# Kernel tuning notes

Measured on AMD Instinct MI355X. Metric: run time of the kernel, lower is better.

Reference implementation:

```python
import jax, jax.numpy as jnp
import numpy as np

NEG_SLOPE = 0.2  # negative_slope of LeakyReLU in GATConv
N_NODES = 50000
N_EDGES = 800000
R = 2
IN_DIM = 128
HID = 32
HEADS = 4
OUT = 32


def setup_inputs() -> dict:
    key = jax.random.key(0)
    ks = jax.random.split(key, 12)
    s = 0.1  # keep pre-activations tame
    x = jax.random.normal(ks[0], (N_NODES, IN_DIM), dtype=jnp.float32)
    W1 = jax.random.normal(ks[1], (R, IN_DIM, HEADS * HID), dtype=jnp.float32) * s
    al1 = jax.random.normal(ks[2], (R, HEADS, HID), dtype=jnp.float32) * s
    ar1 = jax.random.normal(ks[3], (R, HEADS, HID), dtype=jnp.float32) * s
    b1 = jax.random.normal(ks[4], (R, HEADS * HID), dtype=jnp.float32) * s
    W2 = jax.random.normal(ks[5], (R, HEADS * HID, HEADS * OUT), dtype=jnp.float32) * s
    al2 = jax.random.normal(ks[6], (R, HEADS, OUT), dtype=jnp.float32) * s
    ar2 = jax.random.normal(ks[7], (R, HEADS, OUT), dtype=jnp.float32) * s
    b2 = jax.random.normal(ks[8], (R, HEADS * OUT), dtype=jnp.float32) * s
    edges = jax.random.randint(ks[9], (R, 2, N_EDGES), 0, N_NODES, dtype=jnp.int32)
    return {"x": x, "W1": W1, "al1": al1, "ar1": ar1, "b1": b1,
            "W2": W2, "al2": al2, "ar2": ar2, "b2": b2, "edges": edges}


def _gat_rel(h, W, al, ar, src, dst, n):
    """Single-relation GATConv aggregation (no bias/residual/activation)."""
    H, D = al.shape
    feat = (h @ W).reshape(n, H, D)                   # [N,H,D]
    el = jnp.einsum('nhd,hd->nh', feat, al)           # [N,H]
    er = jnp.einsum('nhd,hd->nh', feat, ar)
    e = el[src] + er[dst]                             # [E,H]
    e = jnp.where(e > 0, e, NEG_SLOPE * e)            # LeakyReLU
    # edge softmax over incoming edges of each dst node (numerically stable)
    m = jax.ops.segment_max(e, dst, num_segments=n)
    ex = jnp.exp(e - m[dst])
    denom = jax.ops.segment_sum(ex, dst, num_segments=n)
    alpha = ex / jnp.maximum(denom[dst], 1e-9)        # [E,H]
    msg = alpha[:, :, None] * feat[src]               # [E,H,D]
    return jax.ops.segment_sum(msg, dst, num_segments=n)  # [N,H,D]


def reference(x, W1, al1, ar1, b1, W2, al2, ar2, b2, edges):
    n = x.shape[0]
    r_count = edges.shape[0]
    H1, D1 = al1.shape[1:]
    # --- layer 1: per-relation GATConv (bias + elu inside), sum across relations
    acc = jnp.zeros((n, H1, D1), dtype=x.dtype)
    for r in range(r_count):
        src, dst = edges[r, 0], edges[r, 1]
        o = _gat_rel(x, W1[r], al1[r], ar1[r], src, dst, n)
        acc = acc + jax.nn.elu(o + b1[r].reshape(1, H1, D1))
    h = acc.reshape(n, H1 * D1)                       # flatten heads
    # --- layer 2: residual (identity, since in == heads*out), bias, no activation
    H2, D2 = al2.shape[1:]
    res = h.reshape(n, H2, D2)
    acc2 = jnp.zeros((n, H2, D2), dtype=x.dtype)
    for r in range(r_count):
        src, dst = edges[r, 0], edges[r, 1]
        o = _gat_rel(h, W2[r], al2[r], ar2[r], src, dst, n)
        acc2 = acc2 + o + res + b2[r].reshape(1, H2, D2)
    return acc2.mean(axis=1)                          # mean over heads -> [N, OUT]
```

## Files before the change

### kernel.cpp

```cpp
#include <hip/hip_runtime.h>
#include <math.h>

#define HEADS 4
#define DIM 32
#define FDIM 128
#define EPB 8192
#define BPBSH 8

typedef __attribute__((ext_vector_type(8))) short short8;
typedef __attribute__((ext_vector_type(16))) float float16;

__device__ __forceinline__ unsigned short f2bf(float x) {
  unsigned u = __float_as_uint(x);
  u += 0x7FFFu + ((u >> 16) & 1);
  return (unsigned short)(u >> 16);
}

__global__ void convw_kernel(const float* __restrict__ W1, const float* __restrict__ W2,
                             unsigned short* __restrict__ WT, int R) {
  int idx = blockIdx.x * 256 + threadIdx.x;
  if (idx >= 2 * R * FDIM * FDIM) return;
  int lr = idx >> 14;
  int rem = idx & 16383;
  int n = rem >> 7, k = rem & 127;
  const float* W = (lr < R) ? (W1 + (size_t)lr * FDIM * FDIM)
                            : (W2 + (size_t)(lr - R) * FDIM * FDIM);
  WT[idx] = f2bf(W[k * FDIM + n]);
}

__global__ __launch_bounds__(256) void binA_kernel(const int* __restrict__ edges,
                                                   int* __restrict__ cntA, int E, int BA) {
  __shared__ int hist[256];
  int r = blockIdx.y, blk = blockIdx.x, t = threadIdx.x;
  hist[t] = 0;
  __syncthreads();
  const int* dst = edges + (size_t)r * 2 * E + E;
  int base = blk * EPB;
#pragma unroll
  for (int j = 0; j < EPB / 256; ++j) {
    int e = base + t + j * 256;
    if (e < E) atomicAdd(&hist[dst[e] >> BPBSH], 1);
  }
  __syncthreads();
  cntA[((size_t)r * BA + blk) * 256 + t] = hist[t];
}

__global__ __launch_bounds__(256) void scanA_kernel(int* __restrict__ cntA,
                                                    int* __restrict__ bucketBase,
                                                    int E, int NB, int BA) {
  __shared__ int tot[256];
  __shared__ int basep[257];
  int r = blockIdx.x, b = threadIdx.x;
  int run = 0;
  if (b < NB) {
    for (int blk = 0; blk < BA; ++blk) {
      size_t idx = ((size_t)r * BA + blk) * 256 + b;
      int c = cntA[idx];
      cntA[idx] = run;
      run += c;
    }
  }
  tot[b] = (b < NB) ? run : 0;
  __syncthreads();
  if (b == 0) {
    int acc = 0;
    for (int i = 0; i < NB; ++i) { basep[i] = acc; acc += tot[i]; }
    basep[NB] = acc;
  }
  __syncthreads();
  if (b <= NB) bucketBase[r * 257 + b] = basep[b];
  if (b < NB) {
    int bb = basep[b];
    for (int blk = 0; blk < BA; ++blk)
      cntA[((size_t)r * BA + blk) * 256 + b] += bb;
  }
}

__global__ __launch_bounds__(256) void scatterA_kernel(const int* __restrict__ edges,
    const int* __restrict__ cntA, int2* __restrict__ binned, int E, int BA) {
  __shared__ int cur[256];
  int r = blockIdx.y, blk = blockIdx.x, t = threadIdx.x;
  cur[t] = cntA[((size_t)r * BA + blk) * 256 + t];
  __syncthreads();
  const int* srcp = edges + (size_t)r * 2 * E;
  const int* dstp = srcp + E;
  int2* bout = binned + (size_t)r * E;
  int base = blk * EPB;
#pragma unroll
  for (int j = 0; j < EPB / 256; ++j) {
    int e = base + t + j * 256;
    if (e < E) {
      int d = dstp[e], s = srcp[e];
      int pos = atomicAdd(&cur[d >> BPBSH], 1);
      bout[pos] = make_int2(d, s);
    }
  }
}

__global__ __launch_bounds__(256) void passB_kernel(const int2* __restrict__ binned,
    const int* __restrict__ bucketBase, int* __restrict__ csr, int* __restrict__ indptr,
    int E, int N, int NB) {
  __shared__ int cnt[256];
  __shared__ int off[256];
  __shared__ int cur[256];
  int r = blockIdx.y, b = blockIdx.x, t = threadIdx.x;
  int beg = bucketBase[r * 257 + b];
  int end = bucketBase[r * 257 + b + 1];
  cnt[t] = 0;
  __syncthreads();
  const int2* bin = binned + (size_t)r * E;
  for (int i = beg + t; i < end; i += 256)
    atomicAdd(&cnt[bin[i].x & 255], 1);
  __syncthreads();
  for (int ofs = 1; ofs < 256; ofs <<= 1) {
    int u = (t >= ofs) ? cnt[t - ofs] : 0;
    __syncthreads();
    cnt[t] += u;
    __syncthreads();
  }
  int ex = beg + ((t > 0) ? cnt[t - 1] : 0);
  off[t] = ex;
  cur[t] = ex;
  __syncthreads();
  int node = b * 256 + t;
  if (node < N) indptr[(size_t)r * (N + 1) + node] = off[t];
  if (b == NB - 1 && t == 0) indptr[(size_t)r * (N + 1) + N] = E;
  int* csr_r = csr + (size_t)r * E;
  for (int i = beg + t; i < end; i += 256) {
    int2 p = bin[i];
    int rank = atomicAdd(&cur[p.x & 255], 1);
    csr_r[rank] = p.y;
  }
}

__global__ __launch_bounds__(256) void mm_kernel(const float* __restrict__ A,
    const unsigned short* __restrict__ WTl, const float* __restrict__ al_all,
    const float* __restrict__ ar_all, unsigned short* __restrict__ featb_all,
    float* __restrict__ el_all, float* __restrict__ er_all, int N) {
  __shared__ unsigned short sA[128 * 136];
  __shared__ float sAl[FDIM], sAr[FDIM];
  int r = blockIdx.y;
  const unsigned short* WT = WTl + (size_t)r * FDIM * FDIM;
  int row0 = blockIdx.x * 128;
  int t = threadIdx.x;
  if (t < FDIM) {
    sAl[t] = al_all[r * FDIM + t];
    sAr[t] = ar_all[r * FDIM + t];
  }
#pragma unroll
  for (int it = 0; it < 16; ++it) {
    int idx = t * 4 + it * 1024;
    int row = idx >> 7, k = idx & 127;
    int grow = row0 + row;
    float4 v = make_float4(0.f, 0.f, 0.f, 0.f);
    if (grow < N) v = *(const float4*)(A + (size_t)grow * FDIM + k);
    unsigned short* p = sA + row * 136 + k;
    p[0] = f2bf(v.x); p[1] = f2bf(v.y); p[2] = f2bf(v.z); p[3] = f2bf(v.w);
  }
  __syncthreads();
  int lane = t & 63, w = t >> 6;
  int m = lane & 31, q = lane >> 5;
  float16 acc[4] = {0.f, 0.f, 0.f, 0.f};
#pragma unroll
  for (int kc = 0; kc < 8; ++kc) {
    int ko = kc * 16 + q * 8;
    short8 a = *(const short8*)(sA + (w * 32 + m) * 136 + ko);
#pragma unroll
    for (int nt = 0; nt < 4; ++nt) {
      short8 bb = *(const short8*)(WT + (size_t)(nt * 32 + m) * FDIM + ko);
      acc[nt] = __builtin_amdgcn_mfma_f32_32x32x16_bf16(a, bb, acc[nt], 0, 0, 0);
    }
  }
  __syncthreads();
#pragma unroll
  for (int nt = 0; nt < 4; ++nt) {
#pragma unroll
    for (int reg = 0; reg < 16; ++reg) {
      int rr = (reg & 3) + 8 * (reg >> 2) + 4 * q;
      sA[(w * 32 + rr) * 136 + nt * 32 + m] = f2bf(acc[nt][reg]);
    }
  }
  __syncthreads();
  unsigned short* fb = featb_all + (size_t)r * N * FDIM;
#pragma unroll
  for (int it = 0; it < 8; ++it) {
    int idx = (t + it * 256) * 8;
    int row = idx >> 7, k = idx & 127;
    int grow = row0 + row;
    if (grow < N)
      *(uint4*)(fb + (size_t)grow * FDIM + k) = *(const uint4*)(sA + row * 136 + k);
  }
  int rowc = t >> 1, grow = row0 + rowc;
  if (grow < N) {
    float* elr = el_all + (size_t)r * N * 4;
    float* err_ = er_all + (size_t)r * N * 4;
#pragma unroll
    for (int hh = 0; hh < 2; ++hh) {
      int hd = (t & 1) * 2 + hh;
      const uint4* rp4 = (const uint4*)(sA + rowc * 136 + hd * DIM);
      const float4* alp = (const float4*)(sAl + hd * DIM);
      const float4* arp = (const float4*)(sAr + hd * DIM);
      float sl = 0.f, sr = 0.f;
#pragma unroll
      for (int gq = 0; gq < 4; ++gq) {
        uint4 u = rp4[gq];
        float4 a0 = alp[2 * gq], a1 = alp[2 * gq + 1];
        float4 r0 = arp[2 * gq], r1 = arp[2 * gq + 1];
        unsigned uv[4] = {u.x, u.y, u.z, u.w};
        float fv[8];
#pragma unroll
        for (int j = 0; j < 4; ++j) {
          fv[2 * j] = __uint_as_float(uv[j] << 16);
          fv[2 * j + 1] = __uint_as_float(uv[j] & 0xFFFF0000u);
        }
        sl = fmaf(fv[0], a0.x, sl); sr = fmaf(fv[0], r0.x, sr);
        sl = fmaf(fv[1], a0.y, sl); sr = fmaf(fv[1], r0.y, sr);
        sl = fmaf(fv[2], a0.z, sl); sr = fmaf(fv[2], r0.z, sr);
        sl = fmaf(fv[3], a0.w, sl); sr = fmaf(fv[3], r0.w, sr);
        sl = fmaf(fv[4], a1.x, sl); sr = fmaf(fv[4], r1.x, sr);
        sl = fmaf(fv[5], a1.y, sl); sr = fmaf(fv[5], r1.y, sr);
        sl = fmaf(fv[6], a1.z, sl); sr = fmaf(fv[6], r1.z, sr);
        sl = fmaf(fv[7], a1.w, sl); sr = fmaf(fv[7], r1.w, sr);
      }
      elr[(size_t)grow * 4 + hd] = sl;
      err_[(size_t)grow * 4 + hd] = sr;
    }
  }
}

__global__ __launch_bounds__(256) void agg1_kernel(const unsigned short* __restrict__ featb,
    const float* __restrict__ el, const float* __restrict__ er,
    const int* __restrict__ indptr, const int* __restrict__ csr,
    const float* __restrict__ bias, float* __restrict__ hout, int N, int E, int R) {
  int t = blockIdx.x * 256 + threadIdx.x;
  int node = t >> 3;
  if (node >= N) return;
  int hd = t & 3, sub = (t >> 2) & 1;
  float tot[32];
#pragma unroll
  for (int i = 0; i < 32; ++i) tot[i] = 0.f;
  for (int r = 0; r < R; ++r) {
    const unsigned short* f = featb + (size_t)r * N * FDIM + hd * DIM;
    const float* elr = el + (size_t)r * N * 4;
    const int* csr_r = csr + (size_t)r * E;
    const int* ip = indptr + (size_t)r * (N + 1);
    float er_h = er[(size_t)r * N * 4 + node * 4 + hd];
    int beg = ip[node], end = ip[node + 1];
    float l = 0.f, a[32];
#pragma unroll
    for (int i = 0; i < 32; ++i) a[i] = 0.f;
    for (int i = beg + sub; i < end; i += 2) {
      int s = csr_r[i];
      float ee = elr[s * 4 + hd] + er_h;
      ee = ee > 0.f ? ee : 0.2f * ee;
      float p = __expf(ee);
      const uint4* fp = (const uint4*)(f + (size_t)s * FDIM);
      uint4 u0 = fp[0], u1 = fp[1], u2 = fp[2], u3 = fp[3];
      l += p;
      unsigned uu[16] = {u0.x, u0.y, u0.z, u0.w, u1.x, u1.y, u1.z, u1.w,
                         u2.x, u2.y, u2.z, u2.w, u3.x, u3.y, u3.z, u3.w};
#pragma unroll
      for (int j = 0; j < 16; ++j) {
        float f0 = __uint_as_float(uu[j] << 16);
        float f1 = __uint_as_float(uu[j] & 0xFFFF0000u);
        a[2 * j]     = fmaf(p, f0, a[2 * j]);
        a[2 * j + 1] = fmaf(p, f1, a[2 * j + 1]);
      }
    }
    l += __shfl_xor(l, 4);
#pragma unroll
    for (int i = 0; i < 32; ++i) a[i] += __shfl_xor(a[i], 4);
    float inv = (l > 0.f) ? 1.f / l : 0.f;
    const float4* b4 = (const float4*)(bias + r * FDIM + hd * DIM);
#pragma unroll
    for (int g = 0; g < 8; ++g) {
      float4 bv = b4[g];
      float v0 = a[4 * g] * inv + bv.x;
      float v1 = a[4 * g + 1] * inv + bv.y;
      float v2 = a[4 * g + 2] * inv + bv.z;
      float v3 = a[4 * g + 3] * inv + bv.w;
      tot[4 * g]     += v0 > 0.f ? v0 : __expf(v0) - 1.f;
      tot[4 * g + 1] += v1 > 0.f ? v1 : __expf(v1) - 1.f;
      tot[4 * g + 2] += v2 > 0.f ? v2 : __expf(v2) - 1.f;
      tot[4 * g + 3] += v3 > 0.f ? v3 : __expf(v3) - 1.f;
    }
  }
  if (sub == 0) {
    float4* hp = (float4*)(hout + (size_t)node * FDIM + hd * DIM);
#pragma unroll
    for (int g = 0; g < 8; ++g)
      hp[g] = make_float4(tot[4 * g], tot[4 * g + 1], tot[4 * g + 2], tot[4 * g + 3]);
  }
}

__global__ __launch_bounds__(256) void agg2_kernel(const unsigned short* __restrict__ featb,
    const float* __restrict__ el, const float* __restrict__ er,
    const int* __restrict__ indptr, const int* __restrict__ csr,
    const float* __restrict__ bias, const float* __restrict__ hf,
    float* __restrict__ out, int N, int E, int R) {
  int t = blockIdx.x * 256 + threadIdx.x;
  int node = t >> 3;
  if (node >= N) return;
  int hd = t & 3, sub = (t >> 2) & 1;
  float tot[32];
#pragma unroll
  for (int i = 0; i < 32; ++i) tot[i] = 0.f;
  for (int r = 0; r < R; ++r) {
    const unsigned short* f = featb + (size_t)r * N * FDIM + hd * DIM;
    const float* elr = el + (size_t)r * N * 4;
    const int* csr_r = csr + (size_t)r * E;
    const int* ip = indptr + (size_t)r * (N + 1);
    float er_h = er[(size_t)r * N * 4 + node * 4 + hd];
    int beg = ip[node], end = ip[node + 1];
    float l = 0.f, a[32];
#pragma unroll
    for (int i = 0; i < 32; ++i) a[i] = 0.f;
    for (int i = beg + sub; i < end; i += 2) {
      int s = csr_r[i];
      float ee = elr[s * 4 + hd] + er_h;
      ee = ee > 0.f ? ee : 0.2f * ee;
      float p = __expf(ee);
      const uint4* fp = (const uint4*)(f + (size_t)s * FDIM);
      uint4 u0 = fp[0], u1 = fp[1], u2 = fp[2], u3 = fp[3];
      l += p;
      unsigned uu[16] = {u0.x, u0.y, u0.z, u0.w, u1.x, u1.y, u1.z, u1.w,
                         u2.x, u2.y, u2.z, u2.w, u3.x, u3.y, u3.z, u3.w};
#pragma unroll
      for (int j = 0; j < 16; ++j) {
        float f0 = __uint_as_float(uu[j] << 16);
        float f1 = __uint_as_float(uu[j] & 0xFFFF0000u);
        a[2 * j]     = fmaf(p, f0, a[2 * j]);
        a[2 * j + 1] = fmaf(p, f1, a[2 * j + 1]);
      }
    }
    l += __shfl_xor(l, 4);
#pragma unroll
    for (int i = 0; i < 32; ++i) a[i] += __shfl_xor(a[i], 4);
    float inv = (l > 0.f) ? 1.f / l : 0.f;
    const float4* b4 = (const float4*)(bias + r * FDIM + hd * DIM);
#pragma unroll
    for (int g = 0; g < 8; ++g) {
      float4 bv = b4[g];
      tot[4 * g]     += a[4 * g] * inv + bv.x;
      tot[4 * g + 1] += a[4 * g + 1] * inv + bv.y;
      tot[4 * g + 2] += a[4 * g + 2] * inv + bv.z;
      tot[4 * g + 3] += a[4 * g + 3] * inv + bv.w;
    }
  }
  {
    const float4* rv4 = (const float4*)(hf + (size_t)node * FDIM + hd * DIM);
#pragma unroll
    for (int g = 0; g < 8; ++g) {
      float4 rv = rv4[g];
      tot[4 * g]     += R * rv.x;
      tot[4 * g + 1] += R * rv.y;
      tot[4 * g + 2] += R * rv.z;
      tot[4 * g + 3] += R * rv.w;
    }
  }
#pragma unroll
  for (int i = 0; i < 32; ++i) {
    float v = tot[i];
    v += __shfl_xor(v, 1);
    v += __shfl_xor(v, 2);
    tot[i] = v * 0.25f;
  }
  if (sub == 0) {
    float4* op = (float4*)(out + (size_t)node * 32 + hd * 8);
    op[0] = make_float4(tot[hd * 8], tot[hd * 8 + 1], tot[hd * 8 + 2], tot[hd * 8 + 3]);
    op[1] = make_float4(tot[hd * 8 + 4], tot[hd * 8 + 5], tot[hd * 8 + 6], tot[hd * 8 + 7]);
  }
}

extern "C" void kernel_launch(void* const* d_in, const int* in_sizes, int n_in,
                              void* d_out, int out_size, void* d_ws, size_t ws_size,
                              hipStream_t stream) {
  const float* x   = (const float*)d_in[0];
  const float* W1  = (const float*)d_in[1];
  const float* al1 = (const float*)d_in[2];
  const float* ar1 = (const float*)d_in[3];
  const float* b1  = (const float*)d_in[4];
  const float* W2  = (const float*)d_in[5];
  const float* al2 = (const float*)d_in[6];
  const float* ar2 = (const float*)d_in[7];
  const float* b2  = (const float*)d_in[8];
  const int* edges = (const int*)d_in[9];
  float* out = (float*)d_out;

  const int N = in_sizes[0] / FDIM;
  const int R = in_sizes[1] / (FDIM * FDIM);
  const int E = in_sizes[9] / (2 * R);
  const int BA = (E + EPB - 1) / EPB;
  const int NB = (N + 255) >> BPBSH;

  char* ws = (char*)d_ws;
  size_t off = 0;
  auto alloc = [&](size_t bytes) {
    char* p = ws + off;
    off += (bytes + 255) & ~(size_t)255;
    return p;
  };
  unsigned short* featb = (unsigned short*)alloc((size_t)R * N * FDIM * 2);
  unsigned short* WT    = (unsigned short*)alloc((size_t)2 * R * FDIM * FDIM * 2);
  float* el = (float*)alloc((size_t)R * N * 4 * 4);
  float* er = (float*)alloc((size_t)R * N * 4 * 4);
  float* h  = (float*)alloc((size_t)N * FDIM * 4);
  int* cntA = (int*)alloc((size_t)R * BA * 256 * 4);
  int* bucketBase = (int*)alloc((size_t)R * 257 * 4);
  int2* binned = (int2*)alloc((size_t)R * E * 8);
  int* csr = (int*)alloc((size_t)R * E * 4);
  int* indptr = (int*)alloc((size_t)R * (N + 1) * 4);

  convw_kernel<<<(2 * R * FDIM * FDIM + 255) / 256, 256, 0, stream>>>(W1, W2, WT, R);
  dim3 bgrid(BA, R);
  binA_kernel<<<bgrid, 256, 0, stream>>>(edges, cntA, E, BA);
  scanA_kernel<<<R, 256, 0, stream>>>(cntA, bucketBase, E, NB, BA);
  scatterA_kernel<<<bgrid, 256, 0, stream>>>(edges, cntA, binned, E, BA);
  dim3 pgrid(NB, R);
  passB_kernel<<<pgrid, 256, 0, stream>>>(binned, bucketBase, csr, indptr, E, N, NB);

  dim3 mmgrid((N + 127) / 128, R);
  int agrid = (N * 8 + 255) / 256;

  mm_kernel<<<mmgrid, 256, 0, stream>>>(x, WT, al1, ar1, featb, el, er, N);
  agg1_kernel<<<agrid, 256, 0, stream>>>(featb, el, er, indptr, csr, b1, h, N, E, R);

  mm_kernel<<<mmgrid, 256, 0, stream>>>(h, WT + (size_t)R * FDIM * FDIM, al2, ar2, featb, el, er, N);
  agg2_kernel<<<agrid, 256, 0, stream>>>(featb, el, er, indptr, csr, b2, h, out, N, E, R);
}
```

Measured before the change: 377.7 us.

## Widen aggregation to 4 edge lanes per head, fuse weight conversion into binning

The aggregation kernels now use 16 threads per node instead of 8, so each head's incoming edges are split over 4 lanes, with an extra shuffle-reduction step. The aim is more parallelism and more gathers in flight for the latency-bound edge loop. The weight transpose and bf16 conversion is folded into extra blocks of the binning kernel, which removes one launch. The count table is transposed to a per-bucket row layout so the scan can read rows contiguously and use a parallel prefix sum instead of a serial loop. The cost is twice as many threads each holding 32-float accumulators, plus more shuffles.

New measurement: 387.1 us. 1.02x slower.

```diff
diff --git a/kernel.cpp b/kernel.cpp
--- a/kernel.cpp
+++ b/kernel.cpp
@@ -6,6 +6,7 @@
 #define FDIM 128
 #define EPB 8192
 #define BPBSH 8
+#define WB 16
 
 typedef __attribute__((ext_vector_type(8))) short short8;
 typedef __attribute__((ext_vector_type(16))) float float16;
@@ -16,22 +17,26 @@
   return (unsigned short)(u >> 16);
 }
 
-__global__ void convw_kernel(const float* __restrict__ W1, const float* __restrict__ W2,
-                             unsigned short* __restrict__ WT, int R) {
-  int idx = blockIdx.x * 256 + threadIdx.x;
-  if (idx >= 2 * R * FDIM * FDIM) return;
-  int lr = idx >> 14;
-  int rem = idx & 16383;
-  int n = rem >> 7, k = rem & 127;
-  const float* W = (lr < R) ? (W1 + (size_t)lr * FDIM * FDIM)
-                            : (W2 + (size_t)(lr - R) * FDIM * FDIM);
-  WT[idx] = f2bf(W[k * FDIM + n]);
-}
-
 __global__ __launch_bounds__(256) void binA_kernel(const int* __restrict__ edges,
-                                                   int* __restrict__ cntA, int E, int BA) {
+    int* __restrict__ cntA, const float* __restrict__ W1, const float* __restrict__ W2,
+    unsigned short* __restrict__ WT, int E, int BA, int BAp, int R) {
+  int r = blockIdx.y, blk = blockIdx.x, t = threadIdx.x;
+  if (blk >= BA) {
+    int wb = blk - BA;
+    int base = wb * (32768 / WB);
+#pragma unroll
+    for (int j = 0; j < 32768 / WB; j += 256) {
+      int idx = base + j + t;
+      int layer = idx >> 14;
+      int rem = idx & 16383;
+      int n = rem >> 7, k = rem & 127;
+      const float* W = layer ? (W2 + (size_t)r * FDIM * FDIM)
+                             : (W1 + (size_t)r * FDIM * FDIM);
+      WT[((size_t)(layer * R + r) << 14) + rem] = f2bf(W[k * FDIM + n]);
+    }
+    return;
+  }
   __shared__ int hist[256];
-  int r = blockIdx.y, blk = blockIdx.x, t = threadIdx.x;
   hist[t] = 0;
   __syncthreads();
   const int* dst = edges + (size_t)r * 2 * E + E;
@@ -42,45 +47,43 @@
     if (e < E) atomicAdd(&hist[dst[e] >> BPBSH], 1);
   }
   __syncthreads();
-  cntA[((size_t)r * BA + blk) * 256 + t] = hist[t];
+  cntA[((size_t)r * 256 + t) * BAp + blk] = hist[t];
 }
 
 __global__ __launch_bounds__(256) void scanA_kernel(int* __restrict__ cntA,
-                                                    int* __restrict__ bucketBase,
-                                                    int E, int NB, int BA) {
-  __shared__ int tot[256];
-  __shared__ int basep[257];
+    int* __restrict__ bucketBase, int E, int NB, int BA, int BAp) {
+  __shared__ int stot[256];
   int r = blockIdx.x, b = threadIdx.x;
-  int run = 0;
+  int* row = cntA + ((size_t)r * 256 + b) * BAp;
+  int tot = 0;
+  if (b < NB)
+    for (int blk = 0; blk < BA; ++blk) tot += row[blk];
+  stot[b] = tot;
+  __syncthreads();
+  for (int ofs = 1; ofs < 256; ofs <<= 1) {
+    int u = (b >= ofs) ? stot[b - ofs] : 0;
+    __syncthreads();
+    stot[b] += u;
+    __syncthreads();
+  }
+  int excl = stot[b] - tot;
+  if (b < NB) bucketBase[r * 257 + b] = excl;
+  if (b == 0) bucketBase[r * 257 + NB] = E;
   if (b < NB) {
+    int run = excl;
     for (int blk = 0; blk < BA; ++blk) {
-      size_t idx = ((size_t)r * BA + blk) * 256 + b;
-      int c = cntA[idx];
-      cntA[idx] = run;
+      int c = row[blk];
+      row[blk] = run;
       run += c;
     }
   }
-  tot[b] = (b < NB) ? run : 0;
-  __syncthreads();
-  if (b == 0) {
-    int acc = 0;
-    for (int i = 0; i < NB; ++i) { basep[i] = acc; acc += tot[i]; }
-    basep[NB] = acc;
-  }
-  __syncthreads();
-  if (b <= NB) bucketBase[r * 257 + b] = basep[b];
-  if (b < NB) {
-    int bb = basep[b];
-    for (int blk = 0; blk < BA; ++blk)
-      cntA[((size_t)r * BA + blk) * 256 + b] += bb;
-  }
 }
 
 __global__ __launch_bounds__(256) void scatterA_kernel(const int* __restrict__ edges,
-    const int* __restrict__ cntA, int2* __restrict__ binned, int E, int BA) {
+    const int* __restrict__ cntA, int2* __restrict__ binned, int E, int BA, int BAp) {
   __shared__ int cur[256];
   int r = blockIdx.y, blk = blockIdx.x, t = threadIdx.x;
-  cur[t] = cntA[((size_t)r * BA + blk) * 256 + t];
+  cur[t] = cntA[((size_t)r * 256 + t) * BAp + blk];
   __syncthreads();
   const int* srcp = edges + (size_t)r * 2 * E;
   const int* dstp = srcp + E;
@@ -233,9 +236,9 @@
     const int* __restrict__ indptr, const int* __restrict__ csr,
     const float* __restrict__ bias, float* __restrict__ hout, int N, int E, int R) {
   int t = blockIdx.x * 256 + threadIdx.x;
-  int node = t >> 3;
+  int node = t >> 4;
   if (node >= N) return;
-  int hd = t & 3, sub = (t >> 2) & 1;
+  int hd = t & 3, sub = (t >> 2) & 3;
   float tot[32];
 #pragma unroll
   for (int i = 0; i < 32; ++i) tot[i] = 0.f;
@@ -249,7 +252,7 @@
     float l = 0.f, a[32];
 #pragma unroll
     for (int i = 0; i < 32; ++i) a[i] = 0.f;
-    for (int i = beg + sub; i < end; i += 2) {
+    for (int i = beg + sub; i < end; i += 4) {
       int s = csr_r[i];
       float ee = elr[s * 4 + hd] + er_h;
       ee = ee > 0.f ? ee : 0.2f * ee;
@@ -268,8 +271,14 @@
       }
     }
     l += __shfl_xor(l, 4);
-#pragma unroll
-    for (int i = 0; i < 32; ++i) a[i] += __shfl_xor(a[i], 4);
+    l += __shfl_xor(l, 8);
+#pragma unroll
+    for (int i = 0; i < 32; ++i) {
+      float v = a[i];
+      v += __shfl_xor(v, 4);
+      v += __shfl_xor(v, 8);
+      a[i] = v;
+    }
     float inv = (l > 0.f) ? 1.f / l : 0.f;
     const float4* b4 = (const float4*)(bias + r * FDIM + hd * DIM);
 #pragma unroll
@@ -299,9 +308,9 @@
     const float* __restrict__ bias, const float* __restrict__ hf,
     float* __restrict__ out, int N, int E, int R) {
   int t = blockIdx.x * 256 + threadIdx.x;
-  int node = t >> 3;
+  int node = t >> 4;
   if (node >= N) return;
-  int hd = t & 3, sub = (t >> 2) & 1;
+  int hd = t & 3, sub = (t >> 2) & 3;
   float tot[32];
 #pragma unroll
   for (int i = 0; i < 32; ++i) tot[i] = 0.f;
@@ -315,7 +324,7 @@
     float l = 0.f, a[32];
 #pragma unroll
     for (int i = 0; i < 32; ++i) a[i] = 0.f;
-    for (int i = beg + sub; i < end; i += 2) {
+    for (int i = beg + sub; i < end; i += 4) {
       int s = csr_r[i];
       float ee = elr[s * 4 + hd] + er_h;
       ee = ee > 0.f ? ee : 0.2f * ee;
@@ -334,8 +343,14 @@
       }
     }
     l += __shfl_xor(l, 4);
-#pragma unroll
-    for (int i = 0; i < 32; ++i) a[i] += __shfl_xor(a[i], 4);
+    l += __shfl_xor(l, 8);
+#pragma unroll
+    for (int i = 0; i < 32; ++i) {
+      float v = a[i];
+      v += __shfl_xor(v, 4);
+      v += __shfl_xor(v, 8);
+      a[i] = v;
+    }
     float inv = (l > 0.f) ? 1.f / l : 0.f;
     const float4* b4 = (const float4*)(bias + r * FDIM + hd * DIM);
 #pragma unroll
@@ -391,6 +406,7 @@
   const int R = in_sizes[1] / (FDIM * FDIM);
   const int E = in_sizes[9] / (2 * R);
   const int BA = (E + EPB - 1) / EPB;
+  const int BAp = (BA + 3) & ~3;
   const int NB = (N + 255) >> BPBSH;
 
   char* ws = (char*)d_ws;
@@ -405,22 +421,22 @@
   float* el = (float*)alloc((size_t)R * N * 4 * 4);
   float* er = (float*)alloc((size_t)R * N * 4 * 4);
   float* h  = (float*)alloc((size_t)N * FDIM * 4);
-  int* cntA = (int*)alloc((size_t)R * BA * 256 * 4);
+  int* cntA = (int*)alloc((size_t)R * 256 * BAp * 4);
   int* bucketBase = (int*)alloc((size_t)R * 257 * 4);
   int2* binned = (int2*)alloc((size_t)R * E * 8);
   int* csr = (int*)alloc((size_t)R * E * 4);
   int* indptr = (int*)alloc((size_t)R * (N + 1) * 4);
 
-  convw_kernel<<<(2 * R * FDIM * FDIM + 255) / 256, 256, 0, stream>>>(W1, W2, WT, R);
-  dim3 bgrid(BA, R);
-  binA_kernel<<<bgrid, 256, 0, stream>>>(edges, cntA, E, BA);
-  scanA_kernel<<<R, 256, 0, stream>>>(cntA, bucketBase, E, NB, BA);
-  scatterA_kernel<<<bgrid, 256, 0, stream>>>(edges, cntA, binned, E, BA);
+  dim3 bgrid(BA + WB, R);
+  binA_kernel<<<bgrid, 256, 0, stream>>>(edges, cntA, W1, W2, WT, E, BA, BAp, R);
+  scanA_kernel<<<R, 256, 0, stream>>>(cntA, bucketBase, E, NB, BA, BAp);
+  dim3 sgrid(BA, R);
+  scatterA_kernel<<<sgrid, 256, 0, stream>>>(edges, cntA, binned, E, BA, BAp);
   dim3 pgrid(NB, R);
   passB_kernel<<<pgrid, 256, 0, stream>>>(binned, bucketBase, csr, indptr, E, N, NB);
 
   dim3 mmgrid((N + 127) / 128, R);
-  int agrid = (N * 8 + 255) / 256;
+  int agrid = (N * 16 + 255) / 256;
 
   mm_kernel<<<mmgrid, 256, 0, stream>>>(x, WT, al1, ar1, featb, el, er, N);
   agg1_kernel<<<agrid, 256, 0, stream>>>(featb, el, er, indptr, csr, b1, h, N, E, R);
```
